# Optimization experiments

Hardware: AMD Instinct MI355X
Metric: run time of the kernel (lower is better)

## Reference

```python
import jax, jax.numpy as jnp
import numpy as np

N, R, A, F, T, O = 50000, 5, 8, 128, 2, 128
RADIUS = 1.0

def _template_vertices():
    # polar grid of template vertices in cartesian coords, shape (R, A, 2)
    radii = (np.arange(1, R + 1) / R) * RADIUS
    angles = np.linspace(0.0, 2.0 * np.pi, A, endpoint=False)
    x = radii[:, None] * np.cos(angles)[None, :]
    y = radii[:, None] * np.sin(angles)[None, :]
    return np.stack([x, y], axis=-1)

def _interp_coeffs():
    # Gaussian interpolation coefficients (concrete define_interpolation_coefficients),
    # shape (R, A, R*A), rows normalized -- constant, non-trainable (built in build()).
    v = _template_vertices().reshape(R * A, 2)
    d2 = ((v[:, None, :] - v[None, :, :]) ** 2).sum(-1)
    sigma = RADIUS / R
    w = np.exp(-d2 / (2.0 * sigma ** 2))
    w = w / w.sum(axis=1, keepdims=True)
    return w.reshape(R, A, R * A).astype(np.float32)

def setup_inputs() -> dict:
    key = jax.random.key(0)
    k1, k2, k3, k4, k5 = jax.random.split(key, 5)
    mesh_signal = jax.random.normal(k1, (N, F), dtype=jnp.float32)
    bary_w = jax.random.uniform(k2, (N, R, A, 3), dtype=jnp.float32)
    bary_w = bary_w / bary_w.sum(axis=-1, keepdims=True)  # barycentric weights sum to 1
    bary_idx = jax.random.randint(k3, (N, R, A, 3), 0, N, dtype=jnp.int32)
    glorot = lambda k, shp: jax.random.uniform(
        k, shp, jnp.float32, -1.0, 1.0) * np.sqrt(6.0 / (shp[-1] + shp[-2]))
    template_weights = glorot(k4, (A, T, O, F))  # (n_angular, templates, out, feat)
    bias = glorot(k5, (T, O))
    return {"mesh_signal": mesh_signal, "bary_w": bary_w,
            "template_weights": template_weights, "bias": bias,
            "interp_coeffs": jnp.asarray(_interp_coeffs()),
            "bary_idx": bary_idx}

def reference(mesh_signal, bary_w, template_weights, bias, interp_coeffs, bary_idx):
    # --- patch operator: barycentric gather + interpolation ---
    gathered = mesh_signal[bary_idx]                       # (N,R,A,3,F) irregular gather
    interp = (bary_w[..., None] * gathered).sum(axis=-2)   # (N,R,A,F)
    # prior: mix all R*A template-vertex signals per output template vertex
    sig = interp.reshape(-1, R * A, F)                     # (N,RA,F)
    interp = jnp.einsum('nkf,rak->nraf', sig, interp_coeffs)  # (N,R,A,F)
    # --- fold: all A rotations (rotation_delta=1), vectorized by rolling weights ---
    rots = jnp.arange(0, A, 1)                             # K = A rotations
    idx = (jnp.arange(A)[None, :] + rots[:, None]) % A     # (K,A): roll(interp,+r) == roll(W,-r)
    W_all = template_weights[idx]                          # (K,A,T,O,F)
    # TF adds bias before summing over (R,A) axes -> bias appears R*A times
    z = jnp.einsum('nraf,katof->nkto', interp, W_all) + (R * A) * bias  # (N,K,T,O)
    out = jax.nn.relu(z).sum(axis=2)                       # sum over templates -> (N,K,O)
    return out
```

## Files before the change

kernel.cpp:

```cpp
#include <hip/hip_runtime.h>
#include <hip/hip_bf16.h>
#include <stdint.h>

#define NN 50000
#define RR 5
#define AA 8
#define FF 128
#define TT 2
#define OO 128
#define KDIM 1024
#define NCOLS 2048
#define RA 40
#define NT 32

typedef __attribute__((ext_vector_type(8))) short short8;
typedef __attribute__((ext_vector_type(4))) float f32x4;
typedef __attribute__((ext_vector_type(4))) int i32x4;

__device__ inline void gload_lds16(const void* g, void* l) {
  __builtin_amdgcn_global_load_lds(
      (const __attribute__((address_space(1))) unsigned int*)g,
      (__attribute__((address_space(3))) unsigned int*)l, 16, 0, 0);
}

__global__ void prep_kernel(const float* __restrict__ mesh,
                            const float* __restrict__ coeffs,
                            const float* __restrict__ W,
                            const float* __restrict__ bary_w,
                            const int* __restrict__ bary_idx,
                            __hip_bfloat16* __restrict__ meshq,
                            float* __restrict__ C2,
                            __hip_bfloat16* __restrict__ BmatT,
                            unsigned* __restrict__ packb,
                            int do_pack) {
  int tid = blockIdx.x * blockDim.x + threadIdx.x;
  int stride = gridDim.x * blockDim.x;
  for (int i = tid; i < NN * FF; i += stride) {
    int n = i >> 7, f = i & 127;
    int p = f >> 5, fo = f & 31;
    meshq[((long)p * NN + n) * 32 + fo] = __float2bfloat16(mesh[i]);
  }
  for (int i = tid; i < AA * RA; i += stride) {
    int a = i / RA, k = i % RA;
    float s = 0.f;
    for (int r = 0; r < RR; ++r) s += coeffs[(r * AA + a) * RA + k];
    C2[i] = s;
  }
  for (int i = tid; i < NCOLS * KDIM; i += stride) {
    int c = i >> 10, kf = i & 1023;
    int kr = c >> 8, t = (c >> 7) & 1, o = c & 127;
    int a = kf >> 7, f = kf & 127;
    int arot = (a + kr) & 7;
    BmatT[i] = __float2bfloat16(W[((arot * TT + t) * OO + o) * FF + f]);
  }
  if (do_pack) {
    for (int i = tid; i < NN * 120; i += stride) {
      __hip_bfloat16 h = __float2bfloat16(bary_w[i]);
      unsigned wb = *(unsigned short*)&h;
      packb[i] = ((unsigned)bary_idx[i] << 16) | wb;
    }
  }
}

__global__ __launch_bounds__(256) void s_pass_packed(
    const __hip_bfloat16* __restrict__ meshq,
    const unsigned* __restrict__ packb,
    const float* __restrict__ C2,
    __hip_bfloat16* __restrict__ Sout,
    int p) {
  __shared__ unsigned pk_s[16 * 120];
  __shared__ float c2_s[AA * RA];
  int tid = threadIdx.x;
  long n0 = (long)blockIdx.x * 16;
  const i32x4* psrc = (const i32x4*)(packb + n0 * 120);
  for (int i = tid; i < 480; i += 256) {
    i32x4 v = __builtin_nontemporal_load(psrc + i);
    ((i32x4*)pk_s)[i] = v;
  }
  for (int i = tid; i < AA * RA; i += 256) c2_s[i] = C2[i];
  __syncthreads();

  int g = tid >> 4;
  int fo = tid & 15;
  long n = n0 + g;
  const unsigned* pg = pk_s + g * 120;
  const char* mbase = (const char*)(meshq + (long)p * NN * 32) + fo * 4;

  float sx_acc[AA], sy_acc[AA];
#pragma unroll
  for (int a = 0; a < AA; ++a) { sx_acc[a] = 0.f; sy_acc[a] = 0.f; }

#pragma unroll 2
  for (int k = 0; k < RA; ++k) {
    float sx = 0.f, sy = 0.f;
#pragma unroll
    for (int j = 0; j < 3; ++j) {
      unsigned v = pg[k * 3 + j];
      unsigned row = v >> 16;
      float w = __uint_as_float(v << 16);
      unsigned u = *(const unsigned*)(mbase + (long)row * 64);
      sx += w * __uint_as_float(u << 16);
      sy += w * __uint_as_float(u & 0xffff0000u);
    }
#pragma unroll
    for (int a = 0; a < AA; ++a) {
      float c = c2_s[a * RA + k];
      sx_acc[a] += c * sx;
      sy_acc[a] += c * sy;
    }
  }

  long base = n * KDIM + p * 32 + fo * 2;
#pragma unroll
  for (int a = 0; a < AA; ++a) {
    __hip_bfloat16 hx = __float2bfloat16(sx_acc[a]);
    __hip_bfloat16 hy = __float2bfloat16(sy_acc[a]);
    unsigned u = (unsigned)*(unsigned short*)&hx | ((unsigned)*(unsigned short*)&hy << 16);
    __builtin_nontemporal_store(u, (unsigned*)(Sout + base + a * FF));
  }
}

__global__ __launch_bounds__(256) void s_pass_kernel(
    const __hip_bfloat16* __restrict__ meshq,
    const float* __restrict__ bary_w,
    const int* __restrict__ bary_idx,
    const float* __restrict__ C2,
    __hip_bfloat16* __restrict__ Sout,
    int p) {
  __shared__ float w_s[16 * 120];
  __shared__ int i_s[16 * 120];
  __shared__ float c2_s[AA * RA];
  int tid = threadIdx.x;
  long n0 = (long)blockIdx.x * 16;
  const f32x4* wsrc = (const f32x4*)(bary_w + n0 * 120);
  const i32x4* isrc = (const i32x4*)(bary_idx + n0 * 120);
  for (int i = tid; i < 480; i += 256) {
    f32x4 wv = __builtin_nontemporal_load(wsrc + i);
    ((f32x4*)w_s)[i] = wv;
    i32x4 iv = __builtin_nontemporal_load(isrc + i);
    ((i32x4*)i_s)[i] = iv;
  }
  for (int i = tid; i < AA * RA; i += 256) c2_s[i] = C2[i];
  __syncthreads();
  int g = tid >> 4;
  int fo = tid & 15;
  long n = n0 + g;
  const float* wg = w_s + g * 120;
  const int* ig = i_s + g * 120;
  const char* mbase = (const char*)(meshq + (long)p * NN * 32) + fo * 4;
  float sx_acc[AA], sy_acc[AA];
#pragma unroll
  for (int a = 0; a < AA; ++a) { sx_acc[a] = 0.f; sy_acc[a] = 0.f; }
#pragma unroll 2
  for (int k = 0; k < RA; ++k) {
    float sx = 0.f, sy = 0.f;
#pragma unroll
    for (int j = 0; j < 3; ++j) {
      int row = ig[k * 3 + j];
      unsigned u = *(const unsigned*)(mbase + (long)row * 64);
      float w = wg[k * 3 + j];
      sx += w * __uint_as_float(u << 16);
      sy += w * __uint_as_float(u & 0xffff0000u);
    }
#pragma unroll
    for (int a = 0; a < AA; ++a) {
      float c = c2_s[a * RA + k];
      sx_acc[a] += c * sx;
      sy_acc[a] += c * sy;
    }
  }
  long base = n * KDIM + p * 32 + fo * 2;
#pragma unroll
  for (int a = 0; a < AA; ++a) {
    __hip_bfloat16 hx = __float2bfloat16(sx_acc[a]);
    __hip_bfloat16 hy = __float2bfloat16(sy_acc[a]);
    unsigned u = (unsigned)*(unsigned short*)&hx | ((unsigned)*(unsigned short*)&hy << 16);
    __builtin_nontemporal_store(u, (unsigned*)(Sout + base + a * FF));
  }
}

__global__ __launch_bounds__(512, 1) void gemm_kernel(
    const __hip_bfloat16* __restrict__ S,
    const __hip_bfloat16* __restrict__ BT,
    const float* __restrict__ bias,
    float* __restrict__ out) {
  int bx = blockIdx.x;
  int by = blockIdx.y;
  int kr = by & 7;
  int mt = ((by >> 3) << 3) + bx;
  if (mt >= 196) return;
  int row0 = mt * 256;
  int col0 = kr * 256;

  int tid = threadIdx.x;
  int lane = tid & 63;
  int wid = tid >> 6;
  int wave_m = wid >> 2;
  int wave_n = wid & 3;

  __shared__ __align__(16) char lds[98304];

  f32x4 acc[8][4];
#pragma unroll
  for (int m = 0; m < 8; ++m)
#pragma unroll
    for (int q = 0; q < 4; ++q) acc[m][q] = (f32x4){0.f, 0.f, 0.f, 0.f};

#define STAGE(T, B)                                                         \
  {                                                                         \
    int k0_ = (T) * 32;                                                     \
    char* base_ = lds + (B) * 32768;                                        \
    _Pragma("unroll")                                                       \
    for (int i_ = 0; i_ < 2; ++i_) {                                        \
      int li_ = i_ * 512 + tid;                                             \
      int r_ = li_ >> 2, sp_ = li_ & 3;                                     \
      int sl_ = sp_ ^ ((r_ >> 1) & 3);                                      \
      int row_ = row0 + r_;                                                 \
      if (row_ >= NN) row_ = NN - 1;                                        \
      gload_lds16(S + (long)row_ * KDIM + k0_ + sl_ * 8, base_ + li_ * 16); \
    }                                                                       \
    _Pragma("unroll")                                                       \
    for (int i_ = 0; i_ < 2; ++i_) {                                        \
      int li_ = i_ * 512 + tid;                                             \
      int r_ = li_ >> 2, sp_ = li_ & 3;                                     \
      int sl_ = sp_ ^ ((r_ >> 1) & 3);                                      \
      gload_lds16(BT + (long)(col0 + r_) * KDIM + k0_ + sl_ * 8,            \
                  base_ + 16384 + li_ * 16);                                \
    }                                                                       \
  }

  STAGE(0, 0)
  STAGE(1, 1)

  int bcur = 0, bstage = 2;
  for (int t = 0; t < NT; ++t) {
    if (t < NT - 1) {
      asm volatile("s_waitcnt vmcnt(4)" ::: "memory");
    } else {
      asm volatile("s_waitcnt vmcnt(0)" ::: "memory");
    }
    __builtin_amdgcn_sched_barrier(0);
    __builtin_amdgcn_s_barrier();
    __builtin_amdgcn_sched_barrier(0);
    if (t + 2 < NT) STAGE(t + 2, bstage)
    const char* base = lds + bcur * 32768;
    short8 afr[8], bfr[4];
#pragma unroll
    for (int m = 0; m < 8; ++m) {
      int r = wave_m * 128 + m * 16 + (lane & 15);
      int phys = (lane >> 4) ^ ((r >> 1) & 3);
      afr[m] = *(const short8*)(base + r * 64 + phys * 16);
    }
#pragma unroll
    for (int q = 0; q < 4; ++q) {
      int c = (q >> 1) * 128 + wave_n * 32 + (q & 1) * 16 + (lane & 15);
      int phys = (lane >> 4) ^ ((c >> 1) & 3);
      bfr[q] = *(const short8*)(base + 16384 + c * 64 + phys * 16);
    }
    __builtin_amdgcn_s_setprio(1);
#pragma unroll
    for (int m = 0; m < 8; ++m)
#pragma unroll
      for (int q = 0; q < 4; ++q)
        acc[m][q] = __builtin_amdgcn_mfma_f32_16x16x32_bf16(afr[m], bfr[q], acc[m][q], 0, 0, 0);
    __builtin_amdgcn_s_setprio(0);
    __builtin_amdgcn_sched_barrier(0);
    bcur = (bcur == 2) ? 0 : bcur + 1;
    bstage = (bstage == 2) ? 0 : bstage + 1;
  }

  int olo = wave_n * 32 + (lane & 15);
  float b00 = 40.f * bias[olo];
  float b01 = 40.f * bias[olo + 16];
  float b10 = 40.f * bias[OO + olo];
  float b11 = 40.f * bias[OO + olo + 16];
#pragma unroll
  for (int m = 0; m < 8; ++m) {
#pragma unroll
    for (int i = 0; i < 4; ++i) {
      int node = row0 + wave_m * 128 + m * 16 + (lane >> 4) * 4 + i;
      if (node < NN) {
        float r0 = fmaxf(acc[m][0][i] + b00, 0.f) + fmaxf(acc[m][2][i] + b10, 0.f);
        float r1 = fmaxf(acc[m][1][i] + b01, 0.f) + fmaxf(acc[m][3][i] + b11, 0.f);
        long base = (long)node * 1024 + kr * 128;
        __builtin_nontemporal_store(r0, out + base + olo);
        __builtin_nontemporal_store(r1, out + base + olo + 16);
      }
    }
  }
}

extern "C" void kernel_launch(void* const* d_in, const int* in_sizes, int n_in,
                              void* d_out, int out_size, void* d_ws, size_t ws_size,
                              hipStream_t stream) {
  const float* mesh   = (const float*)d_in[0];
  const float* bary_w = (const float*)d_in[1];
  const float* W      = (const float*)d_in[2];
  const float* bias   = (const float*)d_in[3];
  const float* coeffs = (const float*)d_in[4];
  const int* bidx     = (const int*)d_in[5];
  float* out = (float*)d_out;
  char* ws = (char*)d_ws;

  __hip_bfloat16* meshq = (__hip_bfloat16*)ws;
  float* C2             = (float*)(ws + 12800000);
  __hip_bfloat16* BmatT = (__hip_bfloat16*)(ws + 12801280);
  __hip_bfloat16* Smat  = (__hip_bfloat16*)(ws + 16995584);
  unsigned* packb       = (unsigned*)(ws + 119395584);

  int do_pack = (ws_size >= 143395584UL) ? 1 : 0;

  prep_kernel<<<dim3(2048), dim3(256), 0, stream>>>(mesh, coeffs, W, bary_w, bidx,
                                                    meshq, C2, BmatT, packb, do_pack);
  if (do_pack) {
    for (int p = 0; p < 4; ++p)
      s_pass_packed<<<dim3(3125), dim3(256), 0, stream>>>(meshq, packb, C2, Smat, p);
  } else {
    for (int p = 0; p < 4; ++p)
      s_pass_kernel<<<dim3(3125), dim3(256), 0, stream>>>(meshq, bary_w, bidx, C2, Smat, p);
  }
  gemm_kernel<<<dim3(8, 200), dim3(512), 0, stream>>>(Smat, BmatT, bias, out);
}
```

Baseline: 426.6 us.

## Deepen GEMM pipeline to four LDS stages with split A/B staging per half-step

```diff
diff --git a/kernel.cpp b/kernel.cpp
--- a/kernel.cpp
+++ b/kernel.cpp
@@ -11,7 +11,6 @@
 #define KDIM 1024
 #define NCOLS 2048
 #define RA 40
-#define NT 32
 
 typedef __attribute__((ext_vector_type(8))) short short8;
 typedef __attribute__((ext_vector_type(4))) float f32x4;
@@ -90,7 +89,7 @@
 #pragma unroll
   for (int a = 0; a < AA; ++a) { sx_acc[a] = 0.f; sy_acc[a] = 0.f; }
 
-#pragma unroll 2
+#pragma unroll 5
   for (int k = 0; k < RA; ++k) {
     float sx = 0.f, sy = 0.f;
 #pragma unroll
@@ -151,7 +150,7 @@
   float sx_acc[AA], sy_acc[AA];
 #pragma unroll
   for (int a = 0; a < AA; ++a) { sx_acc[a] = 0.f; sy_acc[a] = 0.f; }
-#pragma unroll 2
+#pragma unroll 5
   for (int k = 0; k < RA; ++k) {
     float sx = 0.f, sy = 0.f;
 #pragma unroll
@@ -180,7 +179,7 @@
 }
 
 __global__ __launch_bounds__(512, 1) void gemm_kernel(
-    const __hip_bfloat16* __restrict__ S,
+    const __hip_bfloat16* __restrict__ Sm,
     const __hip_bfloat16* __restrict__ BT,
     const float* __restrict__ bias,
     float* __restrict__ out) {
@@ -198,7 +197,35 @@
   int wave_m = wid >> 2;
   int wave_n = wid & 3;
 
-  __shared__ __align__(16) char lds[98304];
+  __shared__ __align__(16) char lds[131072];
+
+  long srcA[2], srcB[2];
+  int dstA[2], dstB[2];
+#pragma unroll
+  for (int i = 0; i < 2; ++i) {
+    int li = i * 512 + tid;
+    int r = li >> 2, sp = li & 3;
+    int sl = sp ^ ((r >> 1) & 3);
+    int rowA = row0 + r;
+    if (rowA >= NN) rowA = NN - 1;
+    srcA[i] = (long)rowA * KDIM + sl * 8;
+    dstA[i] = li * 16;
+    srcB[i] = (long)(col0 + r) * KDIM + sl * 8;
+    dstB[i] = 16384 + li * 16;
+  }
+  int offA[8], offB[4];
+#pragma unroll
+  for (int m = 0; m < 8; ++m) {
+    int r = wave_m * 128 + m * 16 + (lane & 15);
+    int phys = (lane >> 4) ^ ((r >> 1) & 3);
+    offA[m] = r * 64 + phys * 16;
+  }
+#pragma unroll
+  for (int q = 0; q < 4; ++q) {
+    int c = (q >> 1) * 128 + wave_n * 32 + (q & 1) * 16 + (lane & 15);
+    int phys = (lane >> 4) ^ ((c >> 1) & 3);
+    offB[q] = 16384 + c * 64 + phys * 16;
+  }
 
   f32x4 acc[8][4];
 #pragma unroll
@@ -206,68 +233,61 @@
 #pragma unroll
     for (int q = 0; q < 4; ++q) acc[m][q] = (f32x4){0.f, 0.f, 0.f, 0.f};
 
-#define STAGE(T, B)                                                         \
-  {                                                                         \
-    int k0_ = (T) * 32;                                                     \
-    char* base_ = lds + (B) * 32768;                                        \
-    _Pragma("unroll")                                                       \
-    for (int i_ = 0; i_ < 2; ++i_) {                                        \
-      int li_ = i_ * 512 + tid;                                             \
-      int r_ = li_ >> 2, sp_ = li_ & 3;                                     \
-      int sl_ = sp_ ^ ((r_ >> 1) & 3);                                      \
-      int row_ = row0 + r_;                                                 \
-      if (row_ >= NN) row_ = NN - 1;                                        \
-      gload_lds16(S + (long)row_ * KDIM + k0_ + sl_ * 8, base_ + li_ * 16); \
-    }                                                                       \
-    _Pragma("unroll")                                                       \
-    for (int i_ = 0; i_ < 2; ++i_) {                                        \
-      int li_ = i_ * 512 + tid;                                             \
-      int r_ = li_ >> 2, sp_ = li_ & 3;                                     \
-      int sl_ = sp_ ^ ((r_ >> 1) & 3);                                      \
-      gload_lds16(BT + (long)(col0 + r_) * KDIM + k0_ + sl_ * 8,            \
-                  base_ + 16384 + li_ * 16);                                \
-    }                                                                       \
-  }
-
-  STAGE(0, 0)
-  STAGE(1, 1)
-
-  int bcur = 0, bstage = 2;
-  for (int t = 0; t < NT; ++t) {
-    if (t < NT - 1) {
-      asm volatile("s_waitcnt vmcnt(4)" ::: "memory");
-    } else {
-      asm volatile("s_waitcnt vmcnt(0)" ::: "memory");
-    }
-    __builtin_amdgcn_sched_barrier(0);
-    __builtin_amdgcn_s_barrier();
-    __builtin_amdgcn_sched_barrier(0);
-    if (t + 2 < NT) STAGE(t + 2, bstage)
-    const char* base = lds + bcur * 32768;
-    short8 afr[8], bfr[4];
-#pragma unroll
-    for (int m = 0; m < 8; ++m) {
-      int r = wave_m * 128 + m * 16 + (lane & 15);
-      int phys = (lane >> 4) ^ ((r >> 1) & 3);
-      afr[m] = *(const short8*)(base + r * 64 + phys * 16);
-    }
-#pragma unroll
-    for (int q = 0; q < 4; ++q) {
-      int c = (q >> 1) * 128 + wave_n * 32 + (q & 1) * 16 + (lane & 15);
-      int phys = (lane >> 4) ^ ((c >> 1) & 3);
-      bfr[q] = *(const short8*)(base + 16384 + c * 64 + phys * 16);
-    }
-    __builtin_amdgcn_s_setprio(1);
-#pragma unroll
-    for (int m = 0; m < 8; ++m)
-#pragma unroll
-      for (int q = 0; q < 4; ++q)
-        acc[m][q] = __builtin_amdgcn_mfma_f32_16x16x32_bf16(afr[m], bfr[q], acc[m][q], 0, 0, 0);
-    __builtin_amdgcn_s_setprio(0);
-    __builtin_amdgcn_sched_barrier(0);
-    bcur = (bcur == 2) ? 0 : bcur + 1;
-    bstage = (bstage == 2) ? 0 : bstage + 1;
-  }
+#define STAGE_A(T)                                                   \
+  {                                                                  \
+    int b_ = ((T) & 3) * 32768;                                      \
+    long k0_ = (long)(T) * 32;                                       \
+    _Pragma("unroll") for (int i_ = 0; i_ < 2; ++i_)                 \
+        gload_lds16(Sm + srcA[i_] + k0_, lds + b_ + dstA[i_]);       \
+  }
+#define STAGE_B(T)                                                   \
+  {                                                                  \
+    int b_ = ((T) & 3) * 32768;                                      \
+    long k0_ = (long)(T) * 32;                                       \
+    _Pragma("unroll") for (int i_ = 0; i_ < 2; ++i_)                 \
+        gload_lds16(BT + srcB[i_] + k0_, lds + b_ + dstB[i_]);       \
+  }
+
+  STAGE_A(0) STAGE_B(0) STAGE_A(1) STAGE_B(1) STAGE_A(2) STAGE_B(2)
+
+#define GSTEP(STP, VMSTR, DOSTAGE)                                            \
+  {                                                                           \
+    const char* cb = lds + ((STP) & 3) * 32768;                               \
+    asm volatile("s_waitcnt " VMSTR ::: "memory");                            \
+    __builtin_amdgcn_sched_barrier(0);                                        \
+    __builtin_amdgcn_s_barrier();                                             \
+    __builtin_amdgcn_sched_barrier(0);                                        \
+    short8 aF[4], bF[4], aG[4];                                               \
+    _Pragma("unroll") for (int m_ = 0; m_ < 4; ++m_)                          \
+        aF[m_] = *(const short8*)(cb + offA[m_]);                             \
+    _Pragma("unroll") for (int q_ = 0; q_ < 4; ++q_)                          \
+        bF[q_] = *(const short8*)(cb + offB[q_]);                             \
+    if (DOSTAGE) STAGE_A((STP) + 3)                                           \
+    __builtin_amdgcn_s_setprio(1);                                            \
+    _Pragma("unroll") for (int m_ = 0; m_ < 4; ++m_)                          \
+        _Pragma("unroll") for (int q_ = 0; q_ < 4; ++q_)                      \
+            acc[m_][q_] = __builtin_amdgcn_mfma_f32_16x16x32_bf16(            \
+                aF[m_], bF[q_], acc[m_][q_], 0, 0, 0);                        \
+    __builtin_amdgcn_s_setprio(0);                                            \
+    __builtin_amdgcn_sched_barrier(0);                                        \
+    __builtin_amdgcn_s_barrier();                                             \
+    __builtin_amdgcn_sched_barrier(0);                                        \
+    _Pragma("unroll") for (int m_ = 0; m_ < 4; ++m_)                          \
+        aG[m_] = *(const short8*)(cb + offA[m_ + 4]);                         \
+    if (DOSTAGE) STAGE_B((STP) + 3)                                           \
+    __builtin_amdgcn_s_setprio(1);                                            \
+    _Pragma("unroll") for (int m_ = 0; m_ < 4; ++m_)                          \
+        _Pragma("unroll") for (int q_ = 0; q_ < 4; ++q_)                      \
+            acc[m_ + 4][q_] = __builtin_amdgcn_mfma_f32_16x16x32_bf16(        \
+                aG[m_], bF[q_], acc[m_ + 4][q_], 0, 0, 0);                    \
+    __builtin_amdgcn_s_setprio(0);                                            \
+    __builtin_amdgcn_sched_barrier(0);                                        \
+  }
+
+  for (int s = 0; s < 29; ++s) GSTEP(s, "vmcnt(8)", 1)
+  GSTEP(29, "vmcnt(8)", 0)
+  GSTEP(30, "vmcnt(4)", 0)
+  GSTEP(31, "vmcnt(0)", 0)
 
   int olo = wave_n * 32 + (lane & 15);
   float b00 = 40.f * bias[olo];
```

After: 435.5 us. 1.02x slower.
